# Optimization experiments

Hardware: AMD Instinct MI355X
Metric: run time of the kernel (lower is better)

Reference implementation:

```python
import jax, jax.numpy as jnp
import numpy as np

EMBED_DIM = 1024
NUM_HEADS = 16
HEAD_DIM = EMBED_DIM // NUM_HEADS
BATCH = 2
SEQ = 2048


def setup_inputs() -> dict:
    key = jax.random.key(0)
    ks = jax.random.split(key, 9)
    scale = 1.0 / np.sqrt(EMBED_DIM)
    return {
        "inputs": jax.random.normal(ks[0], (BATCH, SEQ, EMBED_DIM), jnp.float32),
        "Wq": jax.random.normal(ks[1], (EMBED_DIM, EMBED_DIM), jnp.float32) * scale,
        "bq": jnp.zeros((EMBED_DIM,), jnp.float32),
        "Wk": jax.random.normal(ks[2], (EMBED_DIM, EMBED_DIM), jnp.float32) * scale,
        "bk": jnp.zeros((EMBED_DIM,), jnp.float32),
        "Wv": jax.random.normal(ks[3], (EMBED_DIM, EMBED_DIM), jnp.float32) * scale,
        "bv": jnp.zeros((EMBED_DIM,), jnp.float32),
        "Wo": jax.random.normal(ks[4], (EMBED_DIM, EMBED_DIM), jnp.float32) * scale,
        "bo": jnp.zeros((EMBED_DIM,), jnp.float32),
    }


def reference(inputs, Wq, bq, Wk, bk, Wv, bv, Wo, bo):
    B, S, D = inputs.shape
    H, Dh = NUM_HEADS, HEAD_DIM

    def split_heads(x):  # [B,S,D] -> [B,H,S,Dh]
        return x.reshape(B, S, H, Dh).transpose(0, 2, 1, 3)

    Q = split_heads(inputs @ Wq + bq)
    K = split_heads(inputs @ Wk + bk)
    V = split_heads(inputs @ Wv + bv)

    # naive full-score attention, faithful to the original
    scores = jnp.einsum("bhqd,bhkd->bhqk", Q, K) / jnp.sqrt(jnp.float32(Dh))
    weights = jax.nn.softmax(scores, axis=-1)
    out = jnp.einsum("bhqk,bhkd->bhqd", weights, V)

    concat = out.transpose(0, 2, 1, 3).reshape(B, S, D)
    return concat @ Wo + bo
```

## Files before the change

### kernel.cpp

```cpp
#include <hip/hip_runtime.h>

#define EMBED 1024
#define NHEAD 16
#define HDIM  64
#define BATCH 2
#define SEQ   2048
#define MTOK  (BATCH * SEQ)
#define QSCALE 0.1803368801f

typedef __bf16 bf16x8 __attribute__((ext_vector_type(8)));
typedef float  f32x4  __attribute__((ext_vector_type(4)));

__device__ __forceinline__ unsigned short f2bf(float f) {
  return (unsigned short)((__float_as_uint(f) + 0x8000u) >> 16);
}
__device__ __forceinline__ unsigned int pkbf(float a, float b) {
  unsigned int ua = __float_as_uint(a) + 0x8000u;
  unsigned int ub = __float_as_uint(b) + 0x8000u;
  return __builtin_amdgcn_perm(ub, ua, 0x07060302u);
}

__device__ __forceinline__ void gload_lds16(const unsigned short* g, unsigned short* l) {
  __builtin_amdgcn_global_load_lds((__attribute__((address_space(1))) void*)g,
                                   (__attribute__((address_space(3))) void*)l, 16, 0, 0);
}

__device__ __forceinline__ int kperm(int r) {
  return (r & 32) | (((r >> 2) & 3) << 3) | (((r >> 4) & 1) << 2) | (r & 3);
}

__global__ __launch_bounds__(256)
void prep_k(const float* __restrict__ X, unsigned short* __restrict__ Xbf,
            const float* __restrict__ w0, const float* __restrict__ w1,
            const float* __restrict__ w2, const float* __restrict__ w3,
            unsigned short* __restrict__ t0, unsigned short* __restrict__ t1,
            unsigned short* __restrict__ t2, unsigned short* __restrict__ t3) {
  const int id = blockIdx.x;
  if (id < 4096) {
    int i = id * 256 + threadIdx.x;
    float4 f = reinterpret_cast<const float4*>(X)[i];
    reinterpret_cast<uint2*>(Xbf)[i] = make_uint2(pkbf(f.x, f.y), pkbf(f.z, f.w));
    return;
  }
  const int t = id - 4096;
  const float* s; unsigned short* d;
  switch (t >> 8) {
    case 0: s = w0; d = t0; break;
    case 1: s = w1; d = t1; break;
    case 2: s = w2; d = t2; break;
    default: s = w3; d = t3; break;
  }
  const int tt = t & 255;
  const int k0 = (tt >> 4) * 64, n0 = (tt & 15) * 64;
  __shared__ unsigned short T[64][65];
  for (int i = threadIdx.x; i < 4096; i += 256) {
    int r = i >> 6, c = i & 63;
    T[c][r] = f2bf(s[(size_t)(k0 + r) * EMBED + n0 + c]);
  }
  __syncthreads();
  for (int i = threadIdx.x; i < 4096; i += 256) {
    int r = i >> 6, c = i & 63;
    d[(size_t)(n0 + r) * EMBED + k0 + c] = T[r][c];
  }
}

template<int MODE, int BM>
__global__ void gemm_k(const unsigned short* __restrict__ A,
                       const unsigned short* __restrict__ Bt,
                       const float* __restrict__ b0, const float* __restrict__ b1,
                       const float* __restrict__ b2,
                       unsigned short* __restrict__ oQ, unsigned short* __restrict__ oK,
                       unsigned short* __restrict__ oV, float* __restrict__ oF) {
  constexpr int MI = BM / 32;
  constexpr int NT = EMBED / 32;
  constexpr int LPT = BM / 64 + 2;

  __shared__ unsigned short As[3][BM][32];
  __shared__ unsigned short Bs[3][128][32];

  const int tid = threadIdx.x, lane = tid & 63, wave = tid >> 6;
  const int lr = lane & 15, quad = lane >> 4;
  const int wm = (wave >> 1) * (BM / 2), wn = (wave & 1) * 64;
  const int row0 = blockIdx.x * BM, col0 = blockIdx.y * 128;
  const int srow = lane >> 2, sc = lane & 3;
  const int scsw = (sc ^ ((srow >> 1) & 3)) * 8;
  const int sw = (quad ^ ((lr >> 1) & 3)) * 8;

  const f32x4 fz = {0.f, 0.f, 0.f, 0.f};
  f32x4 acc[MI][4];
#pragma unroll
  for (int i = 0; i < MI; ++i)
#pragma unroll
    for (int j = 0; j < 4; ++j) acc[i][j] = fz;

  auto stage = [&](int bufi, int tt) {
#pragma unroll
    for (int g = 0; g < BM / 64; ++g) {
      int rbase = wave * (BM / 4) + g * 16;
      gload_lds16(&A[(size_t)(row0 + rbase + srow) * EMBED + tt * 32 + scsw],
                  &As[bufi][rbase][0]);
    }
#pragma unroll
    for (int g = 0; g < 2; ++g) {
      int rbase = wave * 32 + g * 16;
      gload_lds16(&Bt[(size_t)(col0 + rbase + srow) * EMBED + tt * 32 + scsw],
                  &Bs[bufi][rbase][0]);
    }
  };

  stage(0, 0);
  stage(1, 1);

  int buf = 0, sb = 2;
  for (int t = 0; t < NT; ++t) {
    if (t < NT - 1)
      asm volatile("s_waitcnt vmcnt(%0)" :: "n"(LPT) : "memory");
    else
      asm volatile("s_waitcnt vmcnt(0)" ::: "memory");
    __builtin_amdgcn_s_barrier();

    bf16x8 af[MI], bv[4];
#pragma unroll
    for (int i = 0; i < MI; ++i)
      af[i] = *reinterpret_cast<const bf16x8*>(&As[buf][wm + i * 16 + lr][sw]);
#pragma unroll
    for (int j = 0; j < 4; ++j)
      bv[j] = *reinterpret_cast<const bf16x8*>(&Bs[buf][wn + j * 16 + lr][sw]);

    __builtin_amdgcn_s_setprio(1);
#pragma unroll
    for (int i = 0; i < MI; ++i)
#pragma unroll
      for (int j = 0; j < 4; ++j)
        acc[i][j] = __builtin_amdgcn_mfma_f32_16x16x32_bf16(af[i], bv[j],
                                                            acc[i][j], 0, 0, 0);
    __builtin_amdgcn_s_setprio(0);

    if (t + 2 < NT) stage(sb, t + 2);
    buf = (buf == 2) ? 0 : buf + 1;
    sb  = (sb  == 2) ? 0 : sb  + 1;
  }

#pragma unroll
  for (int i = 0; i < MI; ++i) {
#pragma unroll
    for (int j = 0; j < 4; ++j) {
      const int col = col0 + wn + j * 16 + lr;
      if (MODE == 1) {
        const float bb = b0[col];
#pragma unroll
        for (int r = 0; r < 4; ++r) {
          const int row = row0 + wm + i * 16 + quad * 4 + r;
          oF[((size_t)row << 10) + col] = acc[i][j][r] + bb;
        }
      } else {
        const int which = col >> 10, cn = col & 1023;
        const float bb = (which == 0 ? b0 : which == 1 ? b1 : b2)[cn];
        const float sscale = (which == 0) ? QSCALE : 1.0f;
        const int h = cn >> 6, dd = cn & 63;
#pragma unroll
        for (int r = 0; r < 4; ++r) {
          const int row = row0 + wm + i * 16 + quad * 4 + r;
          const int b = row >> 11, ss = row & (SEQ - 1);
          const float v = (acc[i][j][r] + bb) * sscale;
          if (which == 0) {
            oQ[((((size_t)b * NHEAD + h) * SEQ + ss) << 6) + dd] = f2bf(v);
          } else if (which == 1) {
            oK[((((size_t)b * NHEAD + h) * SEQ + ss) << 6) + dd] = f2bf(v);
          } else {
            oV[(((size_t)b * NHEAD + h) * HDIM + dd) * SEQ + ss] = f2bf(v);
          }
        }
      }
    }
  }
}

__global__ __launch_bounds__(256, 2)
void attn_k(const unsigned short* __restrict__ Qb,
            const unsigned short* __restrict__ Kb,
            const unsigned short* __restrict__ Vt,
            unsigned short* __restrict__ Ctx) {
  __shared__ unsigned short QPs[128][64];
  __shared__ unsigned short Ks[2][64][64];
  __shared__ unsigned short Vs[2][64][64];
  const int tid = threadIdx.x, lane = tid & 63, wave = tid >> 6;
  const int lr = lane & 15, quad = lane >> 4;
  const int bh = blockIdx.x, qt = blockIdx.y;
  const size_t base = (size_t)bh * SEQ * HDIM;
  const int srow = lane >> 3, sc = lane & 7;
  const int sw0 = (quad ^ (lr & 7)) * 8;
  const int sw1 = ((quad ^ 4) ^ (lr & 7)) * 8;

#pragma unroll
  for (int g = 0; g < 4; ++g) {
    int rbase = wave * 32 + g * 8;
    int row = rbase + srow;
    gload_lds16(&Qb[base + (size_t)(qt * 128 + row) * HDIM + ((sc ^ (row & 7)) * 8)],
                &QPs[rbase][0]);
  }
#pragma unroll
  for (int g = 0; g < 2; ++g) {
    int rbase = wave * 16 + g * 8;
    int row = rbase + srow;
    gload_lds16(&Kb[base + (size_t)kperm(row) * HDIM + ((sc ^ (row & 7)) * 8)],
                &Ks[0][rbase][0]);
    gload_lds16(&Vt[base + (size_t)row * SEQ + ((sc ^ (row & 7)) * 8)],
                &Vs[0][rbase][0]);
  }
  __syncthreads();

  bf16x8 qf[2][2];
#pragma unroll
  for (int g = 0; g < 2; ++g) {
    qf[g][0] = *reinterpret_cast<const bf16x8*>(&QPs[wave * 32 + g * 16 + lr][sw0]);
    qf[g][1] = *reinterpret_cast<const bf16x8*>(&QPs[wave * 32 + g * 16 + lr][sw1]);
  }

  float l_part[2] = {0.f, 0.f};
  const f32x4 fz = {0.f, 0.f, 0.f, 0.f};
  f32x4 oacc[2][4];
#pragma unroll
  for (int g = 0; g < 2; ++g)
#pragma unroll
    for (int d = 0; d < 4; ++d) oacc[g][d] = fz;

  constexpr int NT = SEQ / 64;
  for (int kt = 0;;) {
    const int buf = kt & 1;

    if (kt + 1 < NT) {
#pragma unroll
      for (int g = 0; g < 2; ++g) {
        int rbase = wave * 16 + g * 8;
        int row = rbase + srow;
        gload_lds16(&Kb[base + (size_t)((kt + 1) * 64 + kperm(row)) * HDIM + ((sc ^ (row & 7)) * 8)],
                    &Ks[buf ^ 1][rbase][0]);
        gload_lds16(&Vt[base + (size_t)row * SEQ + (kt + 1) * 64 + ((sc ^ (row & 7)) * 8)],
                    &Vs[buf ^ 1][rbase][0]);
      }
    }

    f32x4 sc4[2][4];
#pragma unroll
    for (int nt = 0; nt < 4; ++nt) {
      bf16x8 kf0 = *reinterpret_cast<const bf16x8*>(&Ks[buf][nt * 16 + lr][sw0]);
      bf16x8 kf1 = *reinterpret_cast<const bf16x8*>(&Ks[buf][nt * 16 + lr][sw1]);
#pragma unroll
      for (int g = 0; g < 2; ++g) {
        f32x4 a = __builtin_amdgcn_mfma_f32_16x16x32_bf16(kf0, qf[g][0], fz, 0, 0, 0);
        sc4[g][nt] = __builtin_amdgcn_mfma_f32_16x16x32_bf16(kf1, qf[g][1], a, 0, 0, 0);
      }
    }

    bf16x8 pf[2][2];
#pragma unroll
    for (int g = 0; g < 2; ++g)
#pragma unroll
      for (int b = 0; b < 2; ++b) {
        float e0 = __builtin_amdgcn_exp2f(sc4[g][2 * b][0]);
        float e1 = __builtin_amdgcn_exp2f(sc4[g][2 * b][1]);
        float e2 = __builtin_amdgcn_exp2f(sc4[g][2 * b][2]);
        float e3 = __builtin_amdgcn_exp2f(sc4[g][2 * b][3]);
        l_part[g] += (e0 + e1) + (e2 + e3);
        float o0 = __builtin_amdgcn_exp2f(sc4[g][2 * b + 1][0]);
        float o1 = __builtin_amdgcn_exp2f(sc4[g][2 * b + 1][1]);
        float o2 = __builtin_amdgcn_exp2f(sc4[g][2 * b + 1][2]);
        float o3 = __builtin_amdgcn_exp2f(sc4[g][2 * b + 1][3]);
        l_part[g] += (o0 + o1) + (o2 + o3);
        union { unsigned int u[4]; bf16x8 v; } pk;
        pk.u[0] = pkbf(e0, e1);
        pk.u[1] = pkbf(e2, e3);
        pk.u[2] = pkbf(o0, o1);
        pk.u[3] = pkbf(o2, o3);
        pf[g][b] = pk.v;
      }

#pragma unroll
    for (int d = 0; d < 4; ++d) {
      bf16x8 vb0 = *reinterpret_cast<const bf16x8*>(&Vs[buf][d * 16 + lr][sw0]);
      bf16x8 vb1 = *reinterpret_cast<const bf16x8*>(&Vs[buf][d * 16 + lr][sw1]);
#pragma unroll
      for (int g = 0; g < 2; ++g) {
        oacc[g][d] = __builtin_amdgcn_mfma_f32_16x16x32_bf16(pf[g][0], vb0, oacc[g][d], 0, 0, 0);
        oacc[g][d] = __builtin_amdgcn_mfma_f32_16x16x32_bf16(pf[g][1], vb1, oacc[g][d], 0, 0, 0);
      }
    }

    if (++kt == NT) break;
    __syncthreads();
  }

#pragma unroll
  for (int g = 0; g < 2; ++g) {
    l_part[g] += __shfl_xor(l_part[g], 16);
    l_part[g] += __shfl_xor(l_part[g], 32);
  }

  const int b = bh >> 4, h = bh & 15;
#pragma unroll
  for (int g = 0; g < 2; ++g) {
    float linv[4];
#pragma unroll
    for (int r = 0; r < 4; ++r) linv[r] = 1.0f / __shfl(l_part[g], quad * 4 + r);
#pragma unroll
    for (int d = 0; d < 4; ++d)
#pragma unroll
      for (int r = 0; r < 4; ++r) {
        const int q = qt * 128 + wave * 32 + g * 16 + quad * 4 + r;
        Ctx[(((size_t)b * SEQ + q) << 10) + h * 64 + d * 16 + lr] =
            f2bf(oacc[g][d][r] * linv[r]);
      }
  }
}

extern "C" void kernel_launch(void* const* d_in, const int* in_sizes, int n_in,
                              void* d_out, int out_size, void* d_ws, size_t ws_size,
                              hipStream_t stream) {
  const float* X  = (const float*)d_in[0];
  const float* Wq = (const float*)d_in[1];
  const float* bq = (const float*)d_in[2];
  const float* Wk = (const float*)d_in[3];
  const float* bk = (const float*)d_in[4];
  const float* Wv = (const float*)d_in[5];
  const float* bv = (const float*)d_in[6];
  const float* Wo = (const float*)d_in[7];
  const float* bo = (const float*)d_in[8];

  unsigned short* ws = (unsigned short*)d_ws;
  const size_t M1 = (size_t)1024 * 1024;
  unsigned short* Xbf = ws;
  unsigned short* WqT = ws + 4 * M1;
  unsigned short* WkT = ws + 5 * M1;
  unsigned short* WvT = ws + 6 * M1;
  unsigned short* WoT = ws + 7 * M1;
  unsigned short* Qb  = ws + 8 * M1;
  unsigned short* Kb  = ws + 12 * M1;
  unsigned short* Vt  = ws + 16 * M1;
  unsigned short* Ctx = ws + 20 * M1;

  prep_k<<<5120, 256, 0, stream>>>(X, Xbf, Wq, Wk, Wv, Wo, WqT, WkT, WvT, WoT);

  gemm_k<0, 128><<<dim3(MTOK / 128, 3072 / 128), 256, 0, stream>>>(
      Xbf, WqT, bq, bk, bv, Qb, Kb, Vt, nullptr);

  attn_k<<<dim3(BATCH * NHEAD, SEQ / 128), 256, 0, stream>>>(Qb, Kb, Vt, Ctx);

  gemm_k<1, 64><<<dim3(MTOK / 64, EMBED / 128), 256, 0, stream>>>(
      Ctx, WoT, bo, nullptr, nullptr, nullptr, nullptr, nullptr, (float*)d_out);
}
```

Measured before the change: 186.6 us.

## Split attention KV range across two blocks and merge partials via atomic flag

The attention kernel now splits the key sequence into two halves with a third grid dimension. Each block writes its unnormalized output accumulator and row sums to a workspace, and the last block to arrive for a query tile (found through an atomic counter) adds in the other half and writes the normalized context. This doubles the grid from 512 to 1024 blocks to fill the GPU better. It also raises the launch-bounds occupancy hint, drops the Q LDS staging in favour of direct global loads, and resets the flags inside the prep kernel. The cost is extra fp32 partial traffic and a fence/atomic merge step, and the merge is only correct if both halves share the same softmax max, apparently a fixed offset.

```diff
diff --git a/kernel.cpp b/kernel.cpp
--- a/kernel.cpp
+++ b/kernel.cpp
@@ -34,9 +34,14 @@
             const float* __restrict__ w0, const float* __restrict__ w1,
             const float* __restrict__ w2, const float* __restrict__ w3,
             unsigned short* __restrict__ t0, unsigned short* __restrict__ t1,
-            unsigned short* __restrict__ t2, unsigned short* __restrict__ t3) {
+            unsigned short* __restrict__ t2, unsigned short* __restrict__ t3,
+            unsigned int* __restrict__ flags) {
   const int id = blockIdx.x;
   if (id < 4096) {
+    if (id == 0) {
+      flags[threadIdx.x] = 0;
+      flags[threadIdx.x + 256] = 0;
+    }
     int i = id * 256 + threadIdx.x;
     float4 f = reinterpret_cast<const float4*>(X)[i];
     reinterpret_cast<uint2*>(Xbf)[i] = make_uint2(pkbf(f.x, f.y), pkbf(f.z, f.w));
@@ -176,46 +181,45 @@
   }
 }
 
-__global__ __launch_bounds__(256, 2)
+__global__ __launch_bounds__(256, 4)
 void attn_k(const unsigned short* __restrict__ Qb,
             const unsigned short* __restrict__ Kb,
             const unsigned short* __restrict__ Vt,
-            unsigned short* __restrict__ Ctx) {
-  __shared__ unsigned short QPs[128][64];
+            unsigned short* __restrict__ Ctx,
+            float* __restrict__ pO,
+            float* __restrict__ pl,
+            unsigned int* __restrict__ flags) {
   __shared__ unsigned short Ks[2][64][64];
   __shared__ unsigned short Vs[2][64][64];
+  __shared__ unsigned int who;
   const int tid = threadIdx.x, lane = tid & 63, wave = tid >> 6;
   const int lr = lane & 15, quad = lane >> 4;
-  const int bh = blockIdx.x, qt = blockIdx.y;
+  const int bh = blockIdx.x, qt = blockIdx.y, kh = blockIdx.z;
   const size_t base = (size_t)bh * SEQ * HDIM;
   const int srow = lane >> 3, sc = lane & 7;
   const int sw0 = (quad ^ (lr & 7)) * 8;
   const int sw1 = ((quad ^ 4) ^ (lr & 7)) * 8;
-
-#pragma unroll
-  for (int g = 0; g < 4; ++g) {
-    int rbase = wave * 32 + g * 8;
-    int row = rbase + srow;
-    gload_lds16(&Qb[base + (size_t)(qt * 128 + row) * HDIM + ((sc ^ (row & 7)) * 8)],
-                &QPs[rbase][0]);
-  }
+  const int lo = kh * 16, hi = lo + 16;
+
+  bf16x8 qf[2][2];
+#pragma unroll
+  for (int g = 0; g < 2; ++g) {
+    const unsigned short* qrow =
+        &Qb[base + (size_t)(qt * 128 + wave * 32 + g * 16 + lr) * HDIM];
+    qf[g][0] = *reinterpret_cast<const bf16x8*>(&qrow[quad * 8]);
+    qf[g][1] = *reinterpret_cast<const bf16x8*>(&qrow[(quad ^ 4) * 8]);
+  }
+
 #pragma unroll
   for (int g = 0; g < 2; ++g) {
     int rbase = wave * 16 + g * 8;
     int row = rbase + srow;
-    gload_lds16(&Kb[base + (size_t)kperm(row) * HDIM + ((sc ^ (row & 7)) * 8)],
+    gload_lds16(&Kb[base + (size_t)(lo * 64 + kperm(row)) * HDIM + ((sc ^ (row & 7)) * 8)],
                 &Ks[0][rbase][0]);
-    gload_lds16(&Vt[base + (size_t)row * SEQ + ((sc ^ (row & 7)) * 8)],
+    gload_lds16(&Vt[base + (size_t)row * SEQ + lo * 64 + ((sc ^ (row & 7)) * 8)],
                 &Vs[0][rbase][0]);
   }
   __syncthreads();
-
-  bf16x8 qf[2][2];
-#pragma unroll
-  for (int g = 0; g < 2; ++g) {
-    qf[g][0] = *reinterpret_cast<const bf16x8*>(&QPs[wave * 32 + g * 16 + lr][sw0]);
-    qf[g][1] = *reinterpret_cast<const bf16x8*>(&QPs[wave * 32 + g * 16 + lr][sw1]);
-  }
 
   float l_part[2] = {0.f, 0.f};
   const f32x4 fz = {0.f, 0.f, 0.f, 0.f};
@@ -225,11 +229,10 @@
 #pragma unroll
     for (int d = 0; d < 4; ++d) oacc[g][d] = fz;
 
-  constexpr int NT = SEQ / 64;
-  for (int kt = 0;;) {
+  for (int kt = lo;;) {
     const int buf = kt & 1;
 
-    if (kt + 1 < NT) {
+    if (kt + 1 < hi) {
 #pragma unroll
       for (int g = 0; g < 2; ++g) {
         int rbase = wave * 16 + g * 8;
@@ -287,7 +290,7 @@
       }
     }
 
-    if (++kt == NT) break;
+    if (++kt == hi) break;
     __syncthreads();
   }
 
@@ -295,6 +298,37 @@
   for (int g = 0; g < 2; ++g) {
     l_part[g] += __shfl_xor(l_part[g], 16);
     l_part[g] += __shfl_xor(l_part[g], 32);
+  }
+
+  const int pair = bh * 16 + qt;
+  float* myO = pO + (size_t)(pair * 2 + kh) * 8192;
+#pragma unroll
+  for (int g = 0; g < 2; ++g)
+#pragma unroll
+    for (int d = 0; d < 4; ++d)
+      *reinterpret_cast<f32x4*>(
+          &myO[(((wave * 8 + g * 4 + d) * 4 + quad) * 16 + lr) * 4]) = oacc[g][d];
+  if (quad == 0) {
+#pragma unroll
+    for (int g = 0; g < 2; ++g)
+      pl[(pair * 2 + kh) * 128 + wave * 32 + g * 16 + lr] = l_part[g];
+  }
+  __threadfence();
+  __syncthreads();
+  if (tid == 0) who = atomicAdd(&flags[pair], 1u);
+  __syncthreads();
+  if (who == 0) return;
+  __threadfence();
+
+  const float* oO = pO + (size_t)(pair * 2 + (1 - kh)) * 8192;
+  const float* ol = pl + (pair * 2 + (1 - kh)) * 128;
+#pragma unroll
+  for (int g = 0; g < 2; ++g) {
+    l_part[g] += ol[wave * 32 + g * 16 + lr];
+#pragma unroll
+    for (int d = 0; d < 4; ++d)
+      oacc[g][d] += *reinterpret_cast<const f32x4*>(
+          &oO[(((wave * 8 + g * 4 + d) * 4 + quad) * 16 + lr) * 4]);
   }
 
   const int b = bh >> 4, h = bh & 15;
@@ -338,13 +372,17 @@
   unsigned short* Kb  = ws + 12 * M1;
   unsigned short* Vt  = ws + 16 * M1;
   unsigned short* Ctx = ws + 20 * M1;
-
-  prep_k<<<5120, 256, 0, stream>>>(X, Xbf, Wq, Wk, Wv, Wo, WqT, WkT, WvT, WoT);
+  float* pO          = (float*)(ws + 24 * M1);
+  float* pl          = (float*)(ws + 40 * M1);
+  unsigned int* flg  = (unsigned int*)(ws + 41 * M1);
+
+  prep_k<<<5120, 256, 0, stream>>>(X, Xbf, Wq, Wk, Wv, Wo, WqT, WkT, WvT, WoT, flg);
 
   gemm_k<0, 128><<<dim3(MTOK / 128, 3072 / 128), 256, 0, stream>>>(
       Xbf, WqT, bq, bk, bv, Qb, Kb, Vt, nullptr);
 
-  attn_k<<<dim3(BATCH * NHEAD, SEQ / 128), 256, 0, stream>>>(Qb, Kb, Vt, Ctx);
+  attn_k<<<dim3(BATCH * NHEAD, SEQ / 128, 2), 256, 0, stream>>>(
+      Qb, Kb, Vt, Ctx, pO, pl, flg);
 
   gemm_k<1, 64><<<dim3(MTOK / 64, EMBED / 128), 256, 0, stream>>>(
       Ctx, WoT, bo, nullptr, nullptr, nullptr, nullptr, nullptr, (float*)d_out);
```

After: 352.9 us. 1.89x slower.

## Replace triple-buffered K=32 GEMM pipeline with single-buffer K=64 loop

Applied to the files above, without the earlier changes.

Drops the three-stage asynchronous LDS pipeline, with its vmcnt waits, in the projection GEMM. It is replaced by a single-buffered loop that loads 64-wide K tiles, waits on two __syncthreads per iteration, and issues two MFMA sub-steps per tile. The LDS swizzle is changed to an 8-way XOR over the 64-wide rows. This halves the number of barrier iterations but removes the overlap of global loads with MFMA compute, so load latency may be exposed.

```diff
diff --git a/kernel.cpp b/kernel.cpp
--- a/kernel.cpp
+++ b/kernel.cpp
@@ -72,19 +72,15 @@
                        unsigned short* __restrict__ oQ, unsigned short* __restrict__ oK,
                        unsigned short* __restrict__ oV, float* __restrict__ oF) {
   constexpr int MI = BM / 32;
-  constexpr int NT = EMBED / 32;
-  constexpr int LPT = BM / 64 + 2;
-
-  __shared__ unsigned short As[3][BM][32];
-  __shared__ unsigned short Bs[3][128][32];
-
+  __shared__ unsigned short As[BM][64];
+  __shared__ unsigned short Bs[128][64];
   const int tid = threadIdx.x, lane = tid & 63, wave = tid >> 6;
   const int lr = lane & 15, quad = lane >> 4;
   const int wm = (wave >> 1) * (BM / 2), wn = (wave & 1) * 64;
   const int row0 = blockIdx.x * BM, col0 = blockIdx.y * 128;
-  const int srow = lane >> 2, sc = lane & 3;
-  const int scsw = (sc ^ ((srow >> 1) & 3)) * 8;
-  const int sw = (quad ^ ((lr >> 1) & 3)) * 8;
+  const int srow = lane >> 3, sc = lane & 7;
+  const int sw0 = (quad ^ (lr & 7)) * 8;
+  const int sw1 = ((quad ^ 4) ^ (lr & 7)) * 8;
 
   const f32x4 fz = {0.f, 0.f, 0.f, 0.f};
   f32x4 acc[MI][4];
@@ -93,52 +89,40 @@
 #pragma unroll
     for (int j = 0; j < 4; ++j) acc[i][j] = fz;
 
-  auto stage = [&](int bufi, int tt) {
-#pragma unroll
-    for (int g = 0; g < BM / 64; ++g) {
-      int rbase = wave * (BM / 4) + g * 16;
-      gload_lds16(&A[(size_t)(row0 + rbase + srow) * EMBED + tt * 32 + scsw],
-                  &As[bufi][rbase][0]);
-    }
-#pragma unroll
-    for (int g = 0; g < 2; ++g) {
-      int rbase = wave * 32 + g * 16;
-      gload_lds16(&Bt[(size_t)(col0 + rbase + srow) * EMBED + tt * 32 + scsw],
-                  &Bs[bufi][rbase][0]);
-    }
-  };
-
-  stage(0, 0);
-  stage(1, 1);
-
-  int buf = 0, sb = 2;
-  for (int t = 0; t < NT; ++t) {
-    if (t < NT - 1)
-      asm volatile("s_waitcnt vmcnt(%0)" :: "n"(LPT) : "memory");
-    else
-      asm volatile("s_waitcnt vmcnt(0)" ::: "memory");
-    __builtin_amdgcn_s_barrier();
-
-    bf16x8 af[MI], bv[4];
-#pragma unroll
-    for (int i = 0; i < MI; ++i)
-      af[i] = *reinterpret_cast<const bf16x8*>(&As[buf][wm + i * 16 + lr][sw]);
-#pragma unroll
-    for (int j = 0; j < 4; ++j)
-      bv[j] = *reinterpret_cast<const bf16x8*>(&Bs[buf][wn + j * 16 + lr][sw]);
-
-    __builtin_amdgcn_s_setprio(1);
-#pragma unroll
-    for (int i = 0; i < MI; ++i)
+  for (int k0 = 0; k0 < EMBED; k0 += 64) {
+#pragma unroll
+    for (int g = 0; g < BM / 32; ++g) {
+      int rbase = wave * (BM / 4) + g * 8;
+      int row = rbase + srow;
+      gload_lds16(&A[(size_t)(row0 + row) * EMBED + k0 + ((sc ^ (row & 7)) * 8)],
+                  &As[rbase][0]);
+    }
+#pragma unroll
+    for (int g = 0; g < 4; ++g) {
+      int rbase = wave * 32 + g * 8;
+      int row = rbase + srow;
+      gload_lds16(&Bt[(size_t)(col0 + row) * EMBED + k0 + ((sc ^ (row & 7)) * 8)],
+                  &Bs[rbase][0]);
+    }
+    __syncthreads();
+#pragma unroll
+    for (int kk = 0; kk < 64; kk += 32) {
+      const int so = (kk == 0) ? sw0 : sw1;
+      bf16x8 af[MI], bv[4];
+#pragma unroll
+      for (int i = 0; i < MI; ++i)
+        af[i] = *reinterpret_cast<const bf16x8*>(&As[wm + i * 16 + lr][so]);
 #pragma unroll
       for (int j = 0; j < 4; ++j)
-        acc[i][j] = __builtin_amdgcn_mfma_f32_16x16x32_bf16(af[i], bv[j],
-                                                            acc[i][j], 0, 0, 0);
-    __builtin_amdgcn_s_setprio(0);
-
-    if (t + 2 < NT) stage(sb, t + 2);
-    buf = (buf == 2) ? 0 : buf + 1;
-    sb  = (sb  == 2) ? 0 : sb  + 1;
+        bv[j] = *reinterpret_cast<const bf16x8*>(&Bs[wn + j * 16 + lr][so]);
+#pragma unroll
+      for (int i = 0; i < MI; ++i)
+#pragma unroll
+        for (int j = 0; j < 4; ++j)
+          acc[i][j] = __builtin_amdgcn_mfma_f32_16x16x32_bf16(af[i], bv[j],
+                                                              acc[i][j], 0, 0, 0);
+    }
+    __syncthreads();
   }
 
 #pragma unroll
```

Result: no change. 184.6 us (-1.1%).
